# Performance work log

Hardware: AMD Instinct MI355X
Metric: run time of the kernel (lower is better)

## Reference

```python
import jax, jax.numpy as jnp
import numpy as np

EMB_DIM = 2048
N_Q_HEADS = 32
N_KV_HEADS = 8
HEAD_DIM = EMB_DIM // N_Q_HEADS  # 64
N_REP = N_Q_HEADS // N_KV_HEADS  # 4
ROPE_BASE = 10000.0


def setup_inputs() -> dict:
    key = jax.random.key(0)
    ks = jax.random.split(key, 9)
    B, T = 2, 2048
    kv_dim = HEAD_DIM * N_KV_HEADS
    s = 0.02
    return {
        "x":  jax.random.normal(ks[0], (B, T, EMB_DIM), jnp.float32),
        "Wq": jax.random.normal(ks[1], (EMB_DIM, EMB_DIM), jnp.float32) * s,
        "bq": jax.random.normal(ks[2], (EMB_DIM,), jnp.float32) * s,
        "Wk": jax.random.normal(ks[3], (kv_dim, EMB_DIM), jnp.float32) * s,
        "bk": jax.random.normal(ks[4], (kv_dim,), jnp.float32) * s,
        "Wv": jax.random.normal(ks[5], (kv_dim, EMB_DIM), jnp.float32) * s,
        "bv": jax.random.normal(ks[6], (kv_dim,), jnp.float32) * s,
        "Wo": jax.random.normal(ks[7], (EMB_DIM, EMB_DIM), jnp.float32) * s,
        "bo": jax.random.normal(ks[8], (EMB_DIM,), jnp.float32) * s,
    }


def _rope_tables(T, D, dtype):
    inv_freq = 1.0 / (ROPE_BASE ** (jnp.arange(0, D, 2, dtype=jnp.float32) / D))
    t = jnp.arange(T, dtype=jnp.float32)
    freqs = jnp.einsum("i,j->ij", t, inv_freq)          # [T, D/2]
    emb = jnp.concatenate([freqs, freqs], axis=-1)       # [T, D]
    # broadcast over batch and heads: [1, T, 1, D]
    return jnp.cos(emb)[None, :, None, :].astype(dtype), jnp.sin(emb)[None, :, None, :].astype(dtype)


def _rotate_half(x):
    x1, x2 = jnp.split(x, 2, axis=-1)
    return jnp.concatenate([-x2, x1], axis=-1)


def reference(x, Wq, bq, Wk, bk, Wv, bv, Wo, bo):
    B, T, C = x.shape
    q = (x @ Wq.T + bq).reshape(B, T, N_Q_HEADS, HEAD_DIM)
    k = (x @ Wk.T + bk).reshape(B, T, N_KV_HEADS, HEAD_DIM)
    v = (x @ Wv.T + bv).reshape(B, T, N_KV_HEADS, HEAD_DIM)

    cos, sin = _rope_tables(T, HEAD_DIM, x.dtype)
    q = q * cos + _rotate_half(q) * sin
    k = k * cos + _rotate_half(k) * sin

    q = q.transpose(0, 2, 1, 3)                          # [B, Hq, T, D]
    k = k.transpose(0, 2, 1, 3)                          # [B, Hkv, T, D]
    v = v.transpose(0, 2, 1, 3)
    # GQA: repeat_interleave kv heads to match query heads
    k = jnp.repeat(k, N_REP, axis=1)                     # [B, Hq, T, D]
    v = jnp.repeat(v, N_REP, axis=1)

    scale = 1.0 / jnp.sqrt(jnp.asarray(HEAD_DIM, x.dtype))
    att = jnp.einsum("bhqd,bhkd->bhqk", q, k) * scale    # [B, Hq, T, T]
    causal = jnp.tril(jnp.ones((T, T), dtype=bool))
    att = jnp.where(causal[None, None], att, -jnp.inf)
    att = jax.nn.softmax(att, axis=-1)

    y = jnp.einsum("bhqk,bhkd->bhqd", att, v)            # [B, Hq, T, D]
    y = y.transpose(0, 2, 1, 3).reshape(B, T, C)
    return y @ Wo.T + bo
```

## Files before the change

### kernel.cpp

```cpp
#include <hip/hip_runtime.h>
#include <hip/hip_bf16.h>
#include <math.h>


typedef __attribute__((ext_vector_type(8))) short short8;
typedef __attribute__((ext_vector_type(4))) float f32x4;

#define MFMA16(a,b,c) __builtin_amdgcn_mfma_f32_16x16x32_bf16((a),(b),(c),0,0,0)
#define QSCALE 0.18033688011112043f
#define NFREQ  (-13.28771237954945f / 32.0f)

__device__ __forceinline__ ushort f2bf(float f) {
  union { float f; unsigned u; } x; x.f = f;
  unsigned r = x.u + 0x7fffu + ((x.u >> 16) & 1u);
  return (ushort)(r >> 16);
}
__device__ __forceinline__ uint pkbf(float a, float b) {
  union { float f; unsigned u; } x, y; x.f = a; y.f = b;
  return ((x.u + 0x8000u) >> 16) | ((y.u + 0x8000u) & 0xffff0000u);
}

__device__ __forceinline__ void g2l16(const void* g, void* l) {
  __builtin_amdgcn_global_load_lds(
      (__attribute__((address_space(1))) void*)g,
      (__attribute__((address_space(3))) void*)l, 16, 0, 0);
}

__global__ void cvt_all(const float* __restrict__ x,  const float* __restrict__ wq,
                        const float* __restrict__ wk, const float* __restrict__ wv,
                        const float* __restrict__ wo,
                        ushort* __restrict__ x_bf, ushort* __restrict__ wqkv,
                        ushort* __restrict__ wo_bf) {
  int i = blockIdx.x * 256 + threadIdx.x;
  const float4* src; ushort* dst; int off;
  if (i < 2097152)      { src = (const float4*)x;  dst = x_bf;             off = i; }
  else if (i < 3145728) { src = (const float4*)wq; dst = wqkv;             off = i - 2097152; }
  else if (i < 3407872) { src = (const float4*)wk; dst = wqkv + 4194304;   off = i - 3145728; }
  else if (i < 3670016) { src = (const float4*)wv; dst = wqkv + 5242880;   off = i - 3407872; }
  else                  { src = (const float4*)wo; dst = wo_bf;            off = i - 3670016; }
  float4 v = src[off];
  ushort4 o;
  o.x = f2bf(v.x); o.y = f2bf(v.y); o.z = f2bf(v.z); o.w = f2bf(v.w);
  ((ushort4*)dst)[off] = o;
}

__global__ __launch_bounds__(256, 3)
void gemm_qkv(const ushort* __restrict__ A, const ushort* __restrict__ Bw,
              const float* __restrict__ bq, const float* __restrict__ bk,
              const float* __restrict__ bv,
              ushort* __restrict__ qr, ushort* __restrict__ kr,
              ushort* __restrict__ vt) {
  const int K = 2048;
  __shared__ ushort As[2][128*32];
  __shared__ ushort Bs[2][128*32];
  const int tid = threadIdx.x;
  const int wave = tid >> 6, lane = tid & 63;
  const int wm = wave >> 1, wn = wave & 1;
  const int quad = lane >> 4, l16 = lane & 15;
  const int swg = (l16 >> 1) & 3;
  const int m0 = blockIdx.y * 128, n0 = blockIdx.x * 128;

  f32x4 acc[4][4] = {};

  auto stage = [&](int buf, int k0) {
#pragma unroll
    for (int i = 0; i < 2; ++i) {
      int cbase = (i*4 + wave) * 64;
      int p = cbase + lane;
      int row = p >> 2, pcb = p & 3;
      int cl = pcb ^ ((row >> 1) & 3);
      g2l16(A  + (size_t)(m0 + row) * K + k0 + cl * 8, As[buf] + (size_t)cbase * 8);
      g2l16(Bw + (size_t)(n0 + row) * K + k0 + cl * 8, Bs[buf] + (size_t)cbase * 8);
    }
  };

  stage(0, 0);
  for (int k0 = 0; k0 < K; k0 += 32) {
    __syncthreads();
    int cur = (k0 >> 5) & 1;
    if (k0 + 32 < K) stage(cur ^ 1, k0 + 32);

    short8 af[4], bfr[4];
#pragma unroll
    for (int mi = 0; mi < 4; ++mi)
      af[mi] = *(const short8*)(As[cur] + (wm*64 + mi*16 + l16)*32 + ((quad ^ swg) * 8));
#pragma unroll
    for (int ni = 0; ni < 4; ++ni)
      bfr[ni] = *(const short8*)(Bs[cur] + (wn*64 + ni*16 + l16)*32 + ((quad ^ swg) * 8));
#pragma unroll
    for (int mi = 0; mi < 4; ++mi)
#pragma unroll
      for (int ni = 0; ni < 4; ++ni)
        acc[mi][ni] = MFMA16(af[mi], bfr[ni], acc[mi][ni]);
  }

  const int bb = m0 >> 11;
  const int tb = (m0 & 2047) + wm*64;

  if (blockIdx.x < 20) {
    const bool isq = blockIdx.x < 16;
    const float scale = isq ? QSCALE : 1.0f;
#pragma unroll
    for (int ni = 0; ni < 2; ++ni) {
      int n = n0 + wn*64 + ni*16 + l16;
      int d = ni*16 + l16;
      float bias1, bias2;
      ushort* dst;
      if (isq) {
        bias1 = bq[n]; bias2 = bq[n + 32];
        dst = qr + ((size_t)(bb*32 + (n >> 6)) * 2048) * 64 + d;
      } else {
        bias1 = bk[n - 2048]; bias2 = bk[n - 2016];
        dst = kr + ((size_t)(bb*8 + ((n >> 6) - 32)) * 2048) * 64 + d;
      }
      float invf = exp2f((float)d * NFREQ);
#pragma unroll
      for (int mi = 0; mi < 4; ++mi) {
#pragma unroll
        for (int r = 0; r < 4; ++r) {
          int t = tb + mi*16 + quad*4 + r;
          float x1 = acc[mi][ni][r]   + bias1;
          float x2 = acc[mi][ni+2][r] + bias2;
          float f = (float)t * invf;
          float sn = __sinf(f), cs = __cosf(f);
          dst[(size_t)t*64]      = f2bf((x1*cs - x2*sn) * scale);
          dst[(size_t)t*64 + 32] = f2bf((x2*cs + x1*sn) * scale);
        }
      }
    }
  } else {
#pragma unroll
    for (int ni = 0; ni < 4; ++ni) {
      int n = n0 + wn*64 + ni*16 + l16;
      int d = ni*16 + l16;
      float bias = bv[n - 2560];
      ushort* dst = vt + ((size_t)(bb*8 + ((n - 2560) >> 6)) * 64 + d) * 2048;
#pragma unroll
      for (int mi = 0; mi < 4; ++mi) {
        int t = tb + mi*16 + quad*4;
        uint2 pk;
        pk.x = (uint)f2bf(acc[mi][ni][0]+bias) | ((uint)f2bf(acc[mi][ni][1]+bias) << 16);
        pk.y = (uint)f2bf(acc[mi][ni][2]+bias) | ((uint)f2bf(acc[mi][ni][3]+bias) << 16);
        *(uint2*)(dst + t) = pk;
      }
    }
  }
}

__global__ __launch_bounds__(256, 3)
void gemm128(const ushort* __restrict__ A, const ushort* __restrict__ Bw,
             const float* __restrict__ b0,
             float* __restrict__ Cout, int M, int N, int K) {
  __shared__ ushort As[2][128*32];
  __shared__ ushort Bs[2][128*32];
  const int tid = threadIdx.x;
  const int wave = tid >> 6, lane = tid & 63;
  const int wm = wave >> 1, wn = wave & 1;
  const int quad = lane >> 4, l16 = lane & 15;
  const int swg = (l16 >> 1) & 3;
  const int m0 = blockIdx.y * 128, n0 = blockIdx.x * 128;

  f32x4 acc[4][4] = {};

  auto stage = [&](int buf, int k0) {
#pragma unroll
    for (int i = 0; i < 2; ++i) {
      int cbase = (i*4 + wave) * 64;
      int p = cbase + lane;
      int row = p >> 2, pcb = p & 3;
      int cl = pcb ^ ((row >> 1) & 3);
      g2l16(A  + (size_t)(m0 + row) * K + k0 + cl * 8, As[buf] + (size_t)cbase * 8);
      g2l16(Bw + (size_t)(n0 + row) * K + k0 + cl * 8, Bs[buf] + (size_t)cbase * 8);
    }
  };

  stage(0, 0);
  for (int k0 = 0; k0 < K; k0 += 32) {
    __syncthreads();
    int cur = (k0 >> 5) & 1;
    if (k0 + 32 < K) stage(cur ^ 1, k0 + 32);

    short8 af[4], bfr[4];
#pragma unroll
    for (int mi = 0; mi < 4; ++mi)
      af[mi] = *(const short8*)(As[cur] + (wm*64 + mi*16 + l16)*32 + ((quad ^ swg) * 8));
#pragma unroll
    for (int ni = 0; ni < 4; ++ni)
      bfr[ni] = *(const short8*)(Bs[cur] + (wn*64 + ni*16 + l16)*32 + ((quad ^ swg) * 8));
#pragma unroll
    for (int mi = 0; mi < 4; ++mi)
#pragma unroll
      for (int ni = 0; ni < 4; ++ni)
        acc[mi][ni] = MFMA16(af[mi], bfr[ni], acc[mi][ni]);
  }

#pragma unroll
  for (int ni = 0; ni < 4; ++ni) {
    int n = n0 + wn*64 + ni*16 + l16;
    float bias = b0[n];
#pragma unroll
    for (int mi = 0; mi < 4; ++mi) {
#pragma unroll
      for (int r = 0; r < 4; ++r) {
        int m = m0 + wm*64 + mi*16 + quad*4 + r;
        Cout[(size_t)m * N + n] = acc[mi][ni][r] + bias;
      }
    }
  }
}

__global__ __launch_bounds__(256, 4)
void attn(const ushort* __restrict__ Q, const ushort* __restrict__ Kb,
          const ushort* __restrict__ Vt, ushort* __restrict__ Y) {
  __shared__ ushort Ks[2][64*64];
  __shared__ ushort Vs[2][64*64];
  __shared__ ushort Ps[4*16*64];
  const int tid = threadIdx.x, wave = tid >> 6, lane = tid & 63;
  const int quad = lane >> 4, l16 = lane & 15;
  const int h = blockIdx.y, b = blockIdx.z;
  const int hk = h >> 2;
  const ushort* Qb = Q  + ((size_t)(b*32 + h)  * 2048) * 64;
  const ushort* Kg = Kb + ((size_t)(b*8 + hk) * 2048) * 64;
  const ushort* Vg = Vt + ((size_t)(b*8 + hk) * 64) * 2048;
  ushort* Pw = Ps + wave * 1024;
  const int sw = l16 & 7;

  auto stage = [&](int buf, int kt) {
#pragma unroll
    for (int i = 0; i < 2; ++i) {
      int cbase = (i*4 + wave) * 64;
      int p = cbase + lane;
      int row = p >> 3, pcb = p & 7;
      int cl = pcb ^ (row & 7);
      g2l16(Kg + (size_t)(kt*64 + row)*64 + cl*8, Ks[buf] + (size_t)cbase*8);
      g2l16(Vg + (size_t)row*2048 + kt*64 + cl*8, Vs[buf] + (size_t)cbase*8);
    }
  };

  for (int pass = 0; pass < 2; ++pass) {
    const int qt = pass ? (31 - blockIdx.x) : blockIdx.x;
    const int q0 = qt * 64;
    const int qrow = q0 + wave*16 + l16;
    short8 qf0 = *(const short8*)(Qb + (size_t)qrow*64 + quad*8);
    short8 qf1 = *(const short8*)(Qb + (size_t)qrow*64 + 32 + quad*8);

    f32x4 o[4] = {};
    f32x4 l4 = {0.f, 0.f, 0.f, 0.f};

    __syncthreads();
    stage(0, 0);

    for (int kt = 0; kt <= qt; ++kt) {
      __syncthreads();
      int cur = kt & 1;
      if (kt < qt) stage(cur ^ 1, kt + 1);

      f32x4 s[4];
#pragma unroll
      for (int kb = 0; kb < 4; ++kb) {
        const ushort* krow = Ks[cur] + (kb*16 + l16)*64;
        short8 kf0 = *(const short8*)(krow + ((quad       ^ sw) * 8));
        short8 kf1 = *(const short8*)(krow + (((4 + quad) ^ sw) * 8));
        f32x4 z = {0.f, 0.f, 0.f, 0.f};
        z = MFMA16(kf0, qf0, z);
        s[kb] = MFMA16(kf1, qf1, z);
      }

      if (kt == qt) {
        int ql = wave*16 + l16;
#pragma unroll
        for (int kb = 0; kb < 4; ++kb) {
          int keyl = kb*16 + quad*4;
#pragma unroll
          for (int r = 0; r < 4; ++r)
            if (keyl + r > ql) s[kb][r] = -INFINITY;
        }
      }

#pragma unroll
      for (int kb = 0; kb < 4; ++kb)
#pragma unroll
        for (int r = 0; r < 4; ++r)
          s[kb][r] = __builtin_amdgcn_exp2f(s[kb][r]);

      l4 += (s[0] + s[1]) + (s[2] + s[3]);

#pragma unroll
      for (int kb = 0; kb < 4; ++kb) {
        uint2 pk;
        pk.x = pkbf(s[kb][0], s[kb][1]);
        pk.y = pkbf(s[kb][2], s[kb][3]);
        int G = (kb*2 + (quad >> 1)) ^ sw;
        *(uint2*)((char*)Pw + l16*128 + G*16 + (quad & 1)*8) = pk;
      }

#pragma unroll
      for (int kc = 0; kc < 2; ++kc) {
        short8 pf = *(const short8*)((char*)Pw + l16*128 + (((kc*4 + quad) ^ sw) * 16));
#pragma unroll
        for (int db = 0; db < 4; ++db) {
          const ushort* vrow = Vs[cur] + (db*16 + l16)*64;
          short8 vf = *(const short8*)(vrow + (((kc*4 + quad) ^ sw) * 8));
          o[db] = MFMA16(vf, pf, o[db]);
        }
      }
    }

    float l = (l4[0] + l4[1]) + (l4[2] + l4[3]);
    l += __shfl_xor(l, 16);
    l += __shfl_xor(l, 32);
    float inv = 1.0f / l;

    int q = q0 + wave*16 + l16;
#pragma unroll
    for (int db = 0; db < 4; ++db) {
      size_t base = ((size_t)(b*2048 + q)) * 2048 + h*64 + db*16 + quad*4;
      ((uint*)Y)[base >> 1]       = pkbf(o[db][0]*inv, o[db][1]*inv);
      ((uint*)Y)[(base >> 1) + 1] = pkbf(o[db][2]*inv, o[db][3]*inv);
    }
  }
}

extern "C" void kernel_launch(void* const* d_in, const int* in_sizes, int n_in,
                              void* d_out, int out_size, void* d_ws, size_t ws_size,
                              hipStream_t stream) {
  (void)in_sizes; (void)n_in; (void)out_size; (void)ws_size;
  const float* x  = (const float*)d_in[0];
  const float* Wq = (const float*)d_in[1];
  const float* bq = (const float*)d_in[2];
  const float* Wk = (const float*)d_in[3];
  const float* bk = (const float*)d_in[4];
  const float* Wv = (const float*)d_in[5];
  const float* bv = (const float*)d_in[6];
  const float* Wo = (const float*)d_in[7];
  const float* bo = (const float*)d_in[8];
  float* out = (float*)d_out;

  ushort* ws    = (ushort*)d_ws;
  ushort* x_bf  = ws;
  ushort* wqkv  = x_bf + 8388608;
  ushort* wo_bf = wqkv + 6291456;
  ushort* qr    = wo_bf + 4194304;
  ushort* kr    = qr + 8388608;
  ushort* vt    = kr + 2097152;
  ushort* Y     = x_bf;

  cvt_all<<<18432, 256, 0, stream>>>(x, Wq, Wk, Wv, Wo, x_bf, wqkv, wo_bf);
  gemm_qkv<<<dim3(24, 32), 256, 0, stream>>>(x_bf, wqkv, bq, bk, bv, qr, kr, vt);
  attn<<<dim3(16, 32, 2), 256, 0, stream>>>(qr, kr, vt, Y);
  gemm128<<<dim3(16, 32), 256, 0, stream>>>(Y, wo_bf, bo, out, 4096, 2048, 2048);
}
```

Baseline: 295.2 us.

## Enlarge QKV GEMM tile to 256x256 with 8 waves and phased pipeline

The QKV projection GEMM moves from 128x128 tiles with 4 waves to 256x256 tiles with 8 waves. Each iteration covers a 64-wide K step split into four phases that interleave global-to-LDS staging with MFMA work, using explicit barriers, waitcnt and setprio. The larger tile gives more data reuse per LDS load and hides load latency, aiming to raise MFMA utilisation. In exchange it launches far fewer blocks (192 on a large-CU device), uses more LDS and registers, and the epilogue index logic had to be remapped, which risks correctness.

```diff
diff --git a/kernel.cpp b/kernel.cpp
--- a/kernel.cpp
+++ b/kernel.cpp
@@ -44,61 +44,105 @@
   ((ushort4*)dst)[off] = o;
 }
 
-__global__ __launch_bounds__(256, 3)
+#define PHASE(curb, ksv, mhv, LOADB, STAGE_CODE, TAIL_CODE)                       \
+  {                                                                               \
+    short8 af[4];                                                                 \
+    _Pragma("unroll")                                                             \
+    for (int mi = 0; mi < 4; ++mi)                                                \
+      af[mi] = *(const short8*)(&As[curb][ksv][(wm*128 + (mhv)*64 + mi*16 + l16)*32 + rdsw]); \
+    if (LOADB) {                                                                  \
+      _Pragma("unroll")                                                           \
+      for (int ni = 0; ni < 4; ++ni)                                              \
+        bfr[ni] = *(const short8*)(&Bs[curb][ksv][(wn*64 + ni*16 + l16)*32 + rdsw]); \
+    }                                                                             \
+    STAGE_CODE;                                                                   \
+    __builtin_amdgcn_s_barrier();                                                 \
+    asm volatile("s_waitcnt lgkmcnt(0)" ::: "memory");                            \
+    __builtin_amdgcn_sched_barrier(0);                                            \
+    __builtin_amdgcn_s_setprio(1);                                                \
+    _Pragma("unroll")                                                             \
+    for (int mi = 0; mi < 4; ++mi) {                                              \
+      _Pragma("unroll")                                                           \
+      for (int ni = 0; ni < 4; ++ni)                                              \
+        acc[(mhv)*4+mi][ni] = MFMA16(af[mi], bfr[ni], acc[(mhv)*4+mi][ni]);       \
+    }                                                                             \
+    __builtin_amdgcn_s_setprio(0);                                                \
+    __builtin_amdgcn_sched_barrier(0);                                            \
+    TAIL_CODE;                                                                    \
+    __builtin_amdgcn_s_barrier();                                                 \
+    __builtin_amdgcn_sched_barrier(0);                                            \
+  }
+
+__global__ __launch_bounds__(512, 2)
 void gemm_qkv(const ushort* __restrict__ A, const ushort* __restrict__ Bw,
               const float* __restrict__ bq, const float* __restrict__ bk,
               const float* __restrict__ bv,
               ushort* __restrict__ qr, ushort* __restrict__ kr,
               ushort* __restrict__ vt) {
-  const int K = 2048;
-  __shared__ ushort As[2][128*32];
-  __shared__ ushort Bs[2][128*32];
+  __shared__ ushort As[2][2][8192];
+  __shared__ ushort Bs[2][2][8192];
   const int tid = threadIdx.x;
   const int wave = tid >> 6, lane = tid & 63;
-  const int wm = wave >> 1, wn = wave & 1;
+  const int wm = wave >> 2, wn = wave & 3;
   const int quad = lane >> 4, l16 = lane & 15;
   const int swg = (l16 >> 1) & 3;
-  const int m0 = blockIdx.y * 128, n0 = blockIdx.x * 128;
-
-  f32x4 acc[4][4] = {};
-
-  auto stage = [&](int buf, int k0) {
+  const int rdsw = ((quad ^ swg) * 8);
+  const int m0 = blockIdx.y * 256, n0 = blockIdx.x * 256;
+
+  f32x4 acc[8][4] = {};
+  short8 bfr[4];
+
+  auto stageA = [&](int buf, int ks, int kcol) {
 #pragma unroll
     for (int i = 0; i < 2; ++i) {
-      int cbase = (i*4 + wave) * 64;
-      int p = cbase + lane;
-      int row = p >> 2, pcb = p & 3;
-      int cl = pcb ^ ((row >> 1) & 3);
-      g2l16(A  + (size_t)(m0 + row) * K + k0 + cl * 8, As[buf] + (size_t)cbase * 8);
-      g2l16(Bw + (size_t)(n0 + row) * K + k0 + cl * 8, Bs[buf] + (size_t)cbase * 8);
+      int seg = i*8 + wave;
+      int p = seg*64 + lane;
+      int row = p >> 2;
+      int cg = (p & 3) ^ ((row >> 1) & 3);
+      g2l16(A + (size_t)(m0 + row) * 2048 + kcol + cg * 8, &As[buf][ks][seg * 512]);
     }
   };
-
-  stage(0, 0);
-  for (int k0 = 0; k0 < K; k0 += 32) {
-    __syncthreads();
-    int cur = (k0 >> 5) & 1;
-    if (k0 + 32 < K) stage(cur ^ 1, k0 + 32);
-
-    short8 af[4], bfr[4];
-#pragma unroll
-    for (int mi = 0; mi < 4; ++mi)
-      af[mi] = *(const short8*)(As[cur] + (wm*64 + mi*16 + l16)*32 + ((quad ^ swg) * 8));
-#pragma unroll
-    for (int ni = 0; ni < 4; ++ni)
-      bfr[ni] = *(const short8*)(Bs[cur] + (wn*64 + ni*16 + l16)*32 + ((quad ^ swg) * 8));
-#pragma unroll
-    for (int mi = 0; mi < 4; ++mi)
-#pragma unroll
-      for (int ni = 0; ni < 4; ++ni)
-        acc[mi][ni] = MFMA16(af[mi], bfr[ni], acc[mi][ni]);
+  auto stageB = [&](int buf, int ks, int kcol) {
+#pragma unroll
+    for (int i = 0; i < 2; ++i) {
+      int seg = i*8 + wave;
+      int p = seg*64 + lane;
+      int row = p >> 2;
+      int cg = (p & 3) ^ ((row >> 1) & 3);
+      g2l16(Bw + (size_t)(n0 + row) * 2048 + kcol + cg * 8, &Bs[buf][ks][seg * 512]);
+    }
+  };
+
+  stageA(0, 0, 0);   stageB(0, 0, 0);
+  stageA(0, 1, 32);  stageB(0, 1, 32);
+  stageA(1, 0, 64);  stageB(1, 0, 64);
+  asm volatile("s_waitcnt vmcnt(4)" ::: "memory");
+  __builtin_amdgcn_s_barrier();
+  __builtin_amdgcn_sched_barrier(0);
+
+  for (int t = 0; t < 32; ++t) {
+    const int cur = t & 1;
+    PHASE(cur, 0, 0, true,
+          { if (t < 31) stageA(cur ^ 1, 1, t*64 + 96); },
+          {});
+    PHASE(cur, 0, 1, false,
+          { if (t < 31) stageB(cur ^ 1, 1, t*64 + 96); },
+          {});
+    PHASE(cur, 1, 0, true,
+          { if (t < 30) stageA(cur, 0, t*64 + 128); },
+          {});
+    PHASE(cur, 1, 1, false,
+          { if (t < 30) stageB(cur, 0, t*64 + 128); },
+          { if (t < 30) { asm volatile("s_waitcnt vmcnt(4)" ::: "memory"); }
+            else        { asm volatile("s_waitcnt vmcnt(0)" ::: "memory"); } });
   }
 
   const int bb = m0 >> 11;
-  const int tb = (m0 & 2047) + wm*64;
-
-  if (blockIdx.x < 20) {
-    const bool isq = blockIdx.x < 16;
+  const int tb = (m0 & 2047) + wm*128;
+  const int bx = blockIdx.x;
+
+  if (bx < 10) {
+    const bool isq = bx < 8;
     const float scale = isq ? QSCALE : 1.0f;
 #pragma unroll
     for (int ni = 0; ni < 2; ++ni) {
@@ -115,7 +159,7 @@
       }
       float invf = exp2f((float)d * NFREQ);
 #pragma unroll
-      for (int mi = 0; mi < 4; ++mi) {
+      for (int mi = 0; mi < 8; ++mi) {
 #pragma unroll
         for (int r = 0; r < 4; ++r) {
           int t = tb + mi*16 + quad*4 + r;
@@ -136,7 +180,7 @@
       float bias = bv[n - 2560];
       ushort* dst = vt + ((size_t)(bb*8 + ((n - 2560) >> 6)) * 64 + d) * 2048;
 #pragma unroll
-      for (int mi = 0; mi < 4; ++mi) {
+      for (int mi = 0; mi < 8; ++mi) {
         int t = tb + mi*16 + quad*4;
         uint2 pk;
         pk.x = (uint)f2bf(acc[mi][ni][0]+bias) | ((uint)f2bf(acc[mi][ni][1]+bias) << 16);
@@ -346,7 +390,7 @@
   ushort* Y     = x_bf;
 
   cvt_all<<<18432, 256, 0, stream>>>(x, Wq, Wk, Wv, Wo, x_bf, wqkv, wo_bf);
-  gemm_qkv<<<dim3(24, 32), 256, 0, stream>>>(x_bf, wqkv, bq, bk, bv, qr, kr, vt);
+  gemm_qkv<<<dim3(12, 16), 512, 0, stream>>>(x_bf, wqkv, bq, bk, bv, qr, kr, vt);
   attn<<<dim3(16, 32, 2), 256, 0, stream>>>(qr, kr, vt, Y);
   gemm128<<<dim3(16, 32), 256, 0, stream>>>(Y, wo_bf, bo, out, 4096, 2048, 2048);
 }
```

After: 306.9 us. +4.0%, slower.

## Triple-buffer GEMM LDS staging and raise wave priority around attention MFMAs

Applied to the files above, without the earlier changes.

Both bf16 GEMM kernels move from double to triple buffering of the A/B LDS tiles, prefetching two k-steps ahead. Each iteration now waits with an explicit vmcnt(4) plus a raw s_barrier instead of a full __syncthreads, so more global-load latency is hidden behind MFMA work. The attention kernel wraps its QK and PV MFMA blocks with s_setprio to favor matrix work over other waves. The extra LDS buffer raises shared memory per block from 32KB to 48KB, which may limit occupancy at launch_bounds 3, and the hand-coded vmcnt counting relies on exactly four outstanding loads per stage.

```diff
diff --git a/kernel.cpp b/kernel.cpp
--- a/kernel.cpp
+++ b/kernel.cpp
@@ -51,8 +51,8 @@
               ushort* __restrict__ qr, ushort* __restrict__ kr,
               ushort* __restrict__ vt) {
   const int K = 2048;
-  __shared__ ushort As[2][128*32];
-  __shared__ ushort Bs[2][128*32];
+  __shared__ ushort As[3][128*32];
+  __shared__ ushort Bs[3][128*32];
   const int tid = threadIdx.x;
   const int wave = tid >> 6, lane = tid & 63;
   const int wm = wave >> 1, wn = wave & 1;
@@ -75,10 +75,14 @@
   };
 
   stage(0, 0);
-  for (int k0 = 0; k0 < K; k0 += 32) {
-    __syncthreads();
-    int cur = (k0 >> 5) & 1;
-    if (k0 + 32 < K) stage(cur ^ 1, k0 + 32);
+  stage(1, 32);
+  int cur = 0, nxt = 2;
+  for (int t = 0; t < 64; ++t) {
+    if (t < 63) asm volatile("s_waitcnt vmcnt(4)" ::: "memory");
+    else        asm volatile("s_waitcnt vmcnt(0)" ::: "memory");
+    __builtin_amdgcn_s_barrier();
+    __builtin_amdgcn_sched_barrier(0);
+    if (t < 62) stage(nxt, t*32 + 64);
 
     short8 af[4], bfr[4];
 #pragma unroll
@@ -92,6 +96,9 @@
 #pragma unroll
       for (int ni = 0; ni < 4; ++ni)
         acc[mi][ni] = MFMA16(af[mi], bfr[ni], acc[mi][ni]);
+
+    cur = (cur == 2) ? 0 : cur + 1;
+    nxt = (nxt == 2) ? 0 : nxt + 1;
   }
 
   const int bb = m0 >> 11;
@@ -151,8 +158,8 @@
 void gemm128(const ushort* __restrict__ A, const ushort* __restrict__ Bw,
              const float* __restrict__ b0,
              float* __restrict__ Cout, int M, int N, int K) {
-  __shared__ ushort As[2][128*32];
-  __shared__ ushort Bs[2][128*32];
+  __shared__ ushort As[3][128*32];
+  __shared__ ushort Bs[3][128*32];
   const int tid = threadIdx.x;
   const int wave = tid >> 6, lane = tid & 63;
   const int wm = wave >> 1, wn = wave & 1;
@@ -174,11 +181,16 @@
     }
   };
 
+  const int NT = K >> 5;
   stage(0, 0);
-  for (int k0 = 0; k0 < K; k0 += 32) {
-    __syncthreads();
-    int cur = (k0 >> 5) & 1;
-    if (k0 + 32 < K) stage(cur ^ 1, k0 + 32);
+  stage(1, 32);
+  int cur = 0, nxt = 2;
+  for (int t = 0; t < NT; ++t) {
+    if (t < NT-1) asm volatile("s_waitcnt vmcnt(4)" ::: "memory");
+    else          asm volatile("s_waitcnt vmcnt(0)" ::: "memory");
+    __builtin_amdgcn_s_barrier();
+    __builtin_amdgcn_sched_barrier(0);
+    if (t < NT-2) stage(nxt, t*32 + 64);
 
     short8 af[4], bfr[4];
 #pragma unroll
@@ -192,6 +204,9 @@
 #pragma unroll
       for (int ni = 0; ni < 4; ++ni)
         acc[mi][ni] = MFMA16(af[mi], bfr[ni], acc[mi][ni]);
+
+    cur = (cur == 2) ? 0 : cur + 1;
+    nxt = (nxt == 2) ? 0 : nxt + 1;
   }
 
 #pragma unroll
@@ -256,6 +271,7 @@
       if (kt < qt) stage(cur ^ 1, kt + 1);
 
       f32x4 s[4];
+      __builtin_amdgcn_s_setprio(1);
 #pragma unroll
       for (int kb = 0; kb < 4; ++kb) {
         const ushort* krow = Ks[cur] + (kb*16 + l16)*64;
@@ -265,6 +281,7 @@
         z = MFMA16(kf0, qf0, z);
         s[kb] = MFMA16(kf1, qf1, z);
       }
+      __builtin_amdgcn_s_setprio(0);
 
       if (kt == qt) {
         int ql = wave*16 + l16;
@@ -294,6 +311,7 @@
         *(uint2*)((char*)Pw + l16*128 + G*16 + (quad & 1)*8) = pk;
       }
 
+      __builtin_amdgcn_s_setprio(1);
 #pragma unroll
       for (int kc = 0; kc < 2; ++kc) {
         short8 pf = *(const short8*)((char*)Pw + l16*128 + (((kc*4 + quad) ^ sw) * 16));
@@ -304,6 +322,7 @@
           o[db] = MFMA16(vf, pf, o[db]);
         }
       }
+      __builtin_amdgcn_s_setprio(0);
     }
 
     float l = (l4[0] + l4[1]) + (l4[2] + l4[3]);
```

Result: no change. 292.8 us (-0.8%).
